# Kernel tuning notes

Hardware: AMD Instinct MI355X
Metric: run time of the kernel (lower is better)

The kernel has to match this reference:

```python
import jax, jax.numpy as jnp
import numpy as np

RATIO = 4
CHANNELS = 256
SIZE = 32

def setup_inputs() -> dict:
    key = jax.random.key(0)
    x = jax.random.normal(key, (16, CHANNELS * RATIO * RATIO, SIZE, SIZE), dtype=jnp.float32)
    return {"input": x}

def reference(input) -> jnp.ndarray:
    # out[b, c, y, x] = in[b, c*r^2 + r*(x%r) + (y%r), y//r, x//r]
    # Equivalent to a depth-to-space with (xr, yr) channel ordering (x-major).
    b, cin, h, w = input.shape
    r = RATIO
    c = cin // (r * r)
    # split channels: [b, c, xr, yr, yb, xb]
    t = input.reshape(b, c, r, r, h, w)
    # -> [b, c, yb, yr, xb, xr]
    t = jnp.transpose(t, (0, 1, 4, 3, 5, 2))
    return t.reshape(b, c, h * r, w * r)
```

## Files before the change

kernel.cpp:

```cpp
#include <hip/hip_runtime.h>
#include <stdint.h>


__global__ __launch_bounds__(256) void ScaleTransfer_kernel(
    const float* __restrict__ in, float* __restrict__ out)
{
    const int blk  = blockIdx.x;
    const int yblk = blk & 15;
    const int bc   = blk >> 4;

    const int t         = threadIdx.x;
    const int row_local = t >> 5;
    const int k         = t & 31;

    const int y  = yblk * 8 + row_local;
    const int yb = y >> 2;
    const int yr = y & 3;

    const int b = bc >> 8;
    const int c = bc & 255;

    const size_t src_off =
        (((size_t)b * 4096 + (size_t)c * 16 + yr) * 32 + yb) * 32 + k;
    const float* src = in + src_off;

    float4 o;
    o.x = src[0 * 4096];
    o.y = src[1 * 4096];
    o.z = src[2 * 4096];
    o.w = src[3 * 4096];

    const size_t dst_off = (((size_t)bc * 128) + y) * 128 + 4 * k;
    *(float4*)(out + dst_off) = o;
}

extern "C" void kernel_launch(void* const* d_in, const int* in_sizes, int n_in,
                              void* d_out, int out_size, void* d_ws, size_t ws_size,
                              hipStream_t stream) {
    const float* in = (const float*)d_in[0];
    float* out = (float*)d_out;
    dim3 grid(16 * 256 * 16);
    dim3 block(256);
    ScaleTransfer_kernel<<<grid, block, 0, stream>>>(in, out);
}
```

Baseline: 427.2 us.

## Stage depth-to-space through LDS with vectorized float4 global loads and stores

Each block now covers a quarter of one (b,c) output plane. It loads 16 input channel slices as float4 vectors into shared memory, synchronizes, then gathers from LDS to build float4 output rows. Before, each thread made four scalar 128-byte-strided loads, so global reads were narrow. Both global reads and writes are now 16-byte vectorized, at the cost of an LDS round trip, a barrier, 16 KB of shared memory per block, and a grid four times smaller.

```diff
diff --git a/kernel.cpp b/kernel.cpp
--- a/kernel.cpp
+++ b/kernel.cpp
@@ -5,33 +5,45 @@
 __global__ __launch_bounds__(256) void ScaleTransfer_kernel(
     const float* __restrict__ in, float* __restrict__ out)
 {
-    const int blk  = blockIdx.x;
-    const int yblk = blk & 15;
-    const int bc   = blk >> 4;
+    __shared__ float lds[16 * 8 * 32];
 
-    const int t         = threadIdx.x;
-    const int row_local = t >> 5;
-    const int k         = t & 31;
+    const int blk = blockIdx.x;
+    const int q   = blk & 3;
+    const int bc  = blk >> 2;
 
-    const int y  = yblk * 8 + row_local;
-    const int yb = y >> 2;
-    const int yr = y & 3;
+    const int t    = threadIdx.x;
+    const int wave = t >> 6;
+    const int lane = t & 63;
 
-    const int b = bc >> 8;
-    const int c = bc & 255;
+    const float* src = in + (size_t)bc * 16384 + (size_t)wave * 1024
+                          + q * 256 + 4 * lane;
+    float4 a0 = *(const float4*)(src + 0 * 4096);
+    float4 a1 = *(const float4*)(src + 1 * 4096);
+    float4 a2 = *(const float4*)(src + 2 * 4096);
+    float4 a3 = *(const float4*)(src + 3 * 4096);
 
-    const size_t src_off =
-        (((size_t)b * 4096 + (size_t)c * 16 + yr) * 32 + yb) * 32 + k;
-    const float* src = in + src_off;
+    float* l = lds + wave * 256 + 4 * lane;
+    *(float4*)(l + 0 * 1024) = a0;
+    *(float4*)(l + 1 * 1024) = a1;
+    *(float4*)(l + 2 * 1024) = a2;
+    *(float4*)(l + 3 * 1024) = a3;
 
-    float4 o;
-    o.x = src[0 * 4096];
-    o.y = src[1 * 4096];
-    o.z = src[2 * 4096];
-    o.w = src[3 * 4096];
+    __syncthreads();
 
-    const size_t dst_off = (((size_t)bc * 128) + y) * 128 + 4 * k;
-    *(float4*)(out + dst_off) = o;
+    float* dst = out + (size_t)bc * 16384 + (size_t)q * 4096 + 4 * t;
+    #pragma unroll
+    for (int i = 0; i < 4; ++i) {
+        const int f  = t + 256 * i;
+        const int yp = f >> 5;
+        const int k  = f & 31;
+        const float* g = lds + (yp & 3) * 256 + (yp >> 2) * 32 + k;
+        float4 o;
+        o.x = g[0 * 1024];
+        o.y = g[1 * 1024];
+        o.z = g[2 * 1024];
+        o.w = g[3 * 1024];
+        *(float4*)(dst + 1024 * i) = o;
+    }
 }
 
 extern "C" void kernel_launch(void* const* d_in, const int* in_sizes, int n_in,
@@ -39,7 +51,7 @@
                               hipStream_t stream) {
     const float* in = (const float*)d_in[0];
     float* out = (float*)d_out;
-    dim3 grid(16 * 256 * 16);
+    dim3 grid(16 * 256 * 4);
     dim3 block(256);
     ScaleTransfer_kernel<<<grid, block, 0, stream>>>(in, out);
 }
```

New measurement: 426.8 us. Within noise of the previous version (-0.1%).
